# Optimization experiments

Hardware: AMD Instinct MI355X
Metric: run time of the kernel (lower is better)

## Reference

```python
import jax, jax.numpy as jnp
import numpy as np

B, S, E = 2, 4096, 512

def setup_inputs() -> dict:
    key = jax.random.key(0)
    kx, kq, kk, kv, ko = jax.random.split(key, 5)
    scale = 1.0 / np.sqrt(E)  # init-style scaling for weights
    return {
        "x": jax.random.normal(kx, (B, S, E), dtype=jnp.float32),
        "Wq": jax.random.normal(kq, (E, E), dtype=jnp.float32) * scale,
        "Wk": jax.random.normal(kk, (E, E), dtype=jnp.float32) * scale,
        "Wv": jax.random.normal(kv, (E, E), dtype=jnp.float32) * scale,
        "Wo": jax.random.normal(ko, (E, E), dtype=jnp.float32) * scale,
        "bo": jnp.zeros((E,), dtype=jnp.float32),
    }

def reference(x, Wq, Wk, Wv, Wo, bo):
    # nn.Linear: y = x @ W.T  (weights stored [out, in])
    q = jnp.einsum("bse,fe->bsf", x, Wq)
    k = jnp.einsum("bse,fe->bsf", x, Wk)
    v = jnp.einsum("bse,fe->bsf", x, Wv)
    inv_scale = 1.0 / jnp.sqrt(jnp.asarray(x.shape[-1], x.dtype))
    scores = jnp.einsum("bqe,bke->bqk", q, k) * inv_scale  # [B,S,S]
    S_len = x.shape[1]
    # torch.triu(ones) keeps j >= i; masked_fill where triu==0 masks j < i
    row = jnp.arange(S_len)[:, None]
    col = jnp.arange(S_len)[None, :]
    keep = col >= row  # [S,S], faithfully anti-causal as in the source
    scores = jnp.where(keep[None, :, :], scores, jnp.asarray(-jnp.inf, scores.dtype))
    attn = jax.nn.softmax(scores, axis=-1)
    # dropout p=0.0 -> identity
    out = jnp.einsum("bqk,bke->bqe", attn, v)
    return jnp.einsum("bse,fe->bsf", out, Wo) + bo
```

## Files before the change

### kernel.cpp

```cpp
#include <hip/hip_runtime.h>
#include <hip/hip_bf16.h>

#define S_LEN 4096
#define E_DIM 512
#define B_DIM 2
#define M_ROWS (B_DIM * S_LEN)

typedef __attribute__((ext_vector_type(8))) short short8;
typedef __attribute__((ext_vector_type(4))) float floatx4;

__device__ __forceinline__ unsigned short f2bf(float f) {
    unsigned u = __float_as_uint(f);
    unsigned r = (u + 0x7fffu + ((u >> 16) & 1u)) >> 16;
    return (unsigned short)r;
}
__device__ __forceinline__ float bf2f(unsigned short u) {
    return __uint_as_float((unsigned)u << 16);
}

__device__ __forceinline__ void async_copy16(unsigned short* lds, const unsigned short* g) {
    auto gp = (const __attribute__((address_space(1))) unsigned int*)g;
    auto lp = (__attribute__((address_space(3))) unsigned int*)lds;
    __builtin_amdgcn_global_load_lds(gp, lp, 16, 0, 0);
}

struct MapArg { unsigned short m[320]; };

__global__ __launch_bounds__(256) void convert_bf16(
    const float* __restrict__ x,  const float* __restrict__ wq,
    const float* __restrict__ wk, const float* __restrict__ wv,
    const float* __restrict__ wo, unsigned short* __restrict__ dst)
{
    long i = (long)blockIdx.x * 1024 + (long)threadIdx.x * 4;
    const float* src; long off;
    if      (i < 4194304) { src = x;  off = i; }
    else if (i < 4456448) { src = wq; off = i - 4194304; }
    else if (i < 4718592) { src = wk; off = i - 4456448; }
    else if (i < 4980736) { src = wv; off = i - 4718592; }
    else                  { src = wo; off = i - 4980736; }
    float4 v = *(const float4*)(src + off);
    ushort4 o;
    o.x = f2bf(v.x); o.y = f2bf(v.y); o.z = f2bf(v.z); o.w = f2bf(v.w);
    *(ushort4*)(dst + i) = o;
}

__device__ __forceinline__ void gemm_core(
    const unsigned short* __restrict__ A, const unsigned short* __restrict__ W,
    void* __restrict__ Cv, const float* __restrict__ bias, int mode,
    int m0, int n0)
{
    __shared__ unsigned short As[128 * 32];
    __shared__ unsigned short Bs[128 * 32];
    const int tid = threadIdx.x;
    const int lane = tid & 63, wave = tid >> 6;
    const int wm = wave >> 1, wn = wave & 1;
    const int q4 = lane >> 4, l16 = lane & 15;

    floatx4 acc[4][4];
#pragma unroll
    for (int i = 0; i < 4; ++i)
#pragma unroll
        for (int j = 0; j < 4; ++j) acc[i][j] = (floatx4){0.f, 0.f, 0.f, 0.f};

    const int srow = lane >> 2;
    const int scol = (lane & 3) * 8;

    for (int k0 = 0; k0 < 512; k0 += 32) {
        async_copy16(&As[(wave * 16) * 32],
                     A + (size_t)(m0 + wave * 16 + srow) * 512 + k0 + scol);
        async_copy16(&As[(64 + wave * 16) * 32],
                     A + (size_t)(m0 + 64 + wave * 16 + srow) * 512 + k0 + scol);
        async_copy16(&Bs[(wave * 16) * 32],
                     W + (size_t)(n0 + wave * 16 + srow) * 512 + k0 + scol);
        async_copy16(&Bs[(64 + wave * 16) * 32],
                     W + (size_t)(n0 + 64 + wave * 16 + srow) * 512 + k0 + scol);
        __syncthreads();
        short8 af[4], bfr[4];
#pragma unroll
        for (int i = 0; i < 4; ++i) {
            af[i]  = *(const short8*)&As[(wm * 64 + i * 16 + l16) * 32 + q4 * 8];
            bfr[i] = *(const short8*)&Bs[(wn * 64 + i * 16 + l16) * 32 + q4 * 8];
        }
#pragma unroll
        for (int i = 0; i < 4; ++i)
#pragma unroll
            for (int j = 0; j < 4; ++j)
                acc[i][j] = __builtin_amdgcn_mfma_f32_16x16x32_bf16(af[i], bfr[j], acc[i][j], 0, 0, 0);
        __syncthreads();
    }

    if (mode == 0) {
        unsigned short* C = (unsigned short*)Cv;
#pragma unroll
        for (int i = 0; i < 4; ++i) {
            int rowb = m0 + wm * 64 + i * 16 + q4 * 4;
#pragma unroll
            for (int j = 0; j < 4; ++j) {
                int col = n0 + wn * 64 + j * 16 + l16;
#pragma unroll
                for (int rg = 0; rg < 4; ++rg)
                    C[(size_t)(rowb + rg) * 512 + col] = f2bf(acc[i][j][rg]);
            }
        }
    } else if (mode == 1) {
        unsigned short* C = (unsigned short*)Cv;
#pragma unroll
        for (int i = 0; i < 4; ++i) {
            int grow = m0 + wm * 64 + i * 16 + q4 * 4;
            int b = grow >> 12, s = grow & 4095;
#pragma unroll
            for (int j = 0; j < 4; ++j) {
                int e = n0 + wn * 64 + j * 16 + l16;
                ushort4 pk;
                pk.x = f2bf(acc[i][j][0]); pk.y = f2bf(acc[i][j][1]);
                pk.z = f2bf(acc[i][j][2]); pk.w = f2bf(acc[i][j][3]);
                *(ushort4*)(C + (size_t)b * 512 * 4096 + (size_t)e * 4096 + s) = pk;
            }
        }
    } else {
        float* C = (float*)Cv;
#pragma unroll
        for (int i = 0; i < 4; ++i) {
            int rowb = m0 + wm * 64 + i * 16 + q4 * 4;
#pragma unroll
            for (int j = 0; j < 4; ++j) {
                int col = n0 + wn * 64 + j * 16 + l16;
                float bv = bias[col];
#pragma unroll
                for (int rg = 0; rg < 4; ++rg)
                    C[(size_t)(rowb + rg) * 512 + col] = acc[i][j][rg] + bv;
            }
        }
    }
}

__global__ __launch_bounds__(256) void gemm_qkv(
    const unsigned short* __restrict__ xb,
    const unsigned short* __restrict__ Wqb, const unsigned short* __restrict__ Wkb,
    const unsigned short* __restrict__ Wvb,
    unsigned short* __restrict__ Qb, unsigned short* __restrict__ Kb,
    unsigned short* __restrict__ Vtb)
{
    const int z = blockIdx.z;
    const unsigned short* W = (z == 0) ? Wqb : (z == 1) ? Wkb : Wvb;
    unsigned short* C = (z == 0) ? Qb : (z == 1) ? Kb : Vtb;
    gemm_core(xb, W, C, nullptr, (z == 2) ? 1 : 0, blockIdx.y * 128, blockIdx.x * 128);
}

__global__ __launch_bounds__(256) void gemm_out(
    const unsigned short* __restrict__ AOb, const unsigned short* __restrict__ Wob,
    const float* __restrict__ bo, float* __restrict__ out)
{
    gemm_core(AOb, Wob, out, bo, 2, blockIdx.y * 128, blockIdx.x * 128);
}

__global__ __launch_bounds__(512, 2) void flash_mfma(
    const unsigned short* __restrict__ Qg, const unsigned short* __restrict__ Kg,
    const unsigned short* __restrict__ Vt,
    unsigned short* __restrict__ Oh, float* __restrict__ Lb, MapArg map)
{
    const int enc = map.m[blockIdx.x];
    const int tile = enc & 63, ch = (enc >> 6) & 3, bb = enc >> 8;
    const int i0 = tile * 64;
    const int lo0 = 1024 * ch, hi = 1024 * ch + 1024;
    const int lo = (i0 > lo0) ? i0 : lo0;

    const int tid = threadIdx.x;
    const int lane = tid & 63, w = tid >> 6;
    const int s = w & 3, h = w >> 2;
    const int q4 = lane >> 4, l16 = lane & 15;
    const float scale = 0.044194173824159216f;
    const float MREF = 4.0f;

    __shared__ float Sred[4][64][36];
    __shared__ unsigned short Plds[64][40];
    __shared__ float Lred[64][8];

    const size_t rowbase = (size_t)bb * S_LEN;
    const size_t vbase   = (size_t)bb * 512 * 4096;

    short8 aq[4][4];
#pragma unroll
    for (int mg = 0; mg < 4; ++mg)
#pragma unroll
        for (int ks = 0; ks < 4; ++ks)
            aq[mg][ks] = *(const short8*)(Qg + (rowbase + i0 + mg * 16 + l16) * 512
                                          + s * 128 + ks * 32 + q4 * 8);

    floatx4 oacc[4][4];
#pragma unroll
    for (int mg = 0; mg < 4; ++mg)
#pragma unroll
        for (int nc = 0; nc < 4; ++nc) oacc[mg][nc] = (floatx4){0.f, 0.f, 0.f, 0.f};

    const int r = tid >> 3;
    const int g = tid & 7;
    float l_acc = 0.f;

    auto step = [&](int j0, short8 (&bkc)[4], short8 (&bkn)[4], int jn) {
        short8 vf[4];
#pragma unroll
        for (int nc = 0; nc < 4; ++nc)
            vf[nc] = *(const short8*)(Vt + vbase
                + (size_t)(w * 64 + nc * 16 + l16) * 4096 + j0 + q4 * 8);
#pragma unroll
        for (int ks = 0; ks < 4; ++ks)
            bkn[ks] = *(const short8*)(Kg + (rowbase + jn + h * 16 + l16) * 512
                                       + s * 128 + ks * 32 + q4 * 8);
        floatx4 sf[4];
#pragma unroll
        for (int mg = 0; mg < 4; ++mg) sf[mg] = (floatx4){0.f, 0.f, 0.f, 0.f};
#pragma unroll
        for (int ks = 0; ks < 4; ++ks)
#pragma unroll
            for (int mg = 0; mg < 4; ++mg)
                sf[mg] = __builtin_amdgcn_mfma_f32_16x16x32_bf16(
                    bkc[ks], aq[mg][ks], sf[mg], 0, 0, 0);
#pragma unroll
        for (int mg = 0; mg < 4; ++mg)
            *(floatx4*)&Sred[s][mg * 16 + l16][h * 16 + q4 * 4] = sf[mg];
        __syncthreads();

        float4 a0 = *(const float4*)&Sred[0][r][4 * g];
        float4 a1 = *(const float4*)&Sred[1][r][4 * g];
        float4 a2 = *(const float4*)&Sred[2][r][4 * g];
        float4 a3 = *(const float4*)&Sred[3][r][4 * g];
        float sv[4] = { a0.x + a1.x + a2.x + a3.x, a0.y + a1.y + a2.y + a3.y,
                        a0.z + a1.z + a2.z + a3.z, a0.w + a1.w + a2.w + a3.w };
        ushort4 pk;
        float p0, p1, p2, p3;
        {
            int key = j0 + 4 * g;
            int row = i0 + r;
            p0 = (key + 0 >= row) ? __expf(sv[0] * scale - MREF) : 0.f;
            p1 = (key + 1 >= row) ? __expf(sv[1] * scale - MREF) : 0.f;
            p2 = (key + 2 >= row) ? __expf(sv[2] * scale - MREF) : 0.f;
            p3 = (key + 3 >= row) ? __expf(sv[3] * scale - MREF) : 0.f;
        }
        l_acc += p0 + p1 + p2 + p3;
        pk.x = f2bf(p0); pk.y = f2bf(p1); pk.z = f2bf(p2); pk.w = f2bf(p3);
        *(ushort4*)&Plds[r][4 * g] = pk;
        __syncthreads();

        short8 ap[4];
#pragma unroll
        for (int mg = 0; mg < 4; ++mg)
            ap[mg] = *(const short8*)&Plds[mg * 16 + l16][q4 * 8];
#pragma unroll
        for (int mg = 0; mg < 4; ++mg)
#pragma unroll
            for (int nc = 0; nc < 4; ++nc)
                oacc[mg][nc] = __builtin_amdgcn_mfma_f32_16x16x32_bf16(
                    ap[mg], vf[nc], oacc[mg][nc], 0, 0, 0);
    };

    short8 bkA[4], bkB[4];
    int j0 = hi - 32;
#pragma unroll
    for (int ks = 0; ks < 4; ++ks)
        bkA[ks] = *(const short8*)(Kg + (rowbase + j0 + h * 16 + l16) * 512
                                   + s * 128 + ks * 32 + q4 * 8);
    while (j0 >= lo) {
        int jn = (j0 - 32 >= lo) ? j0 - 32 : lo;
        step(j0, bkA, bkB, jn);
        j0 -= 32;
        if (j0 < lo) break;
        jn = (j0 - 32 >= lo) ? j0 - 32 : lo;
        step(j0, bkB, bkA, jn);
        j0 -= 32;
    }
    __syncthreads();

    const int baseArr = (ch == 0) ? 0 : (ch == 1) ? 32 : (ch == 2) ? 96 : 192;
    const int slot = baseArr + bb * 16 * (ch + 1) + tile;

    Lred[r][g] = l_acc;
    __syncthreads();
    if (tid < 64) {
        float sum = 0.f;
#pragma unroll
        for (int gg = 0; gg < 8; ++gg) sum += Lred[tid][gg];
        Lb[(size_t)slot * 64 + tid] = sum;
    }

    unsigned short* Op = Oh + (size_t)slot * 64 * 512;
#pragma unroll
    for (int mg = 0; mg < 4; ++mg)
#pragma unroll
        for (int nc = 0; nc < 4; ++nc)
#pragma unroll
            for (int rg = 0; rg < 4; ++rg)
                Op[(size_t)(mg * 16 + q4 * 4 + rg) * 512 + w * 64 + nc * 16 + l16]
                    = f2bf(oacc[mg][nc][rg]);
}

__global__ __launch_bounds__(256) void flash_merge(
    const unsigned short* __restrict__ Oh, const float* __restrict__ Lb,
    unsigned short* __restrict__ AO)
{
    const int row = blockIdx.x;
    const int c = threadIdx.x * 2;
    const int bb = row >> 12, i = row & 4095;
    const int t = i >> 6, ri = i & 63;
    const int chmin = i >> 10;
    float lsum = 0.f, v0 = 0.f, v1 = 0.f;
#pragma unroll
    for (int ch = 0; ch < 4; ++ch) {
        if (ch < chmin) continue;
        int baseArr = (ch == 0) ? 0 : (ch == 1) ? 32 : (ch == 2) ? 96 : 192;
        int slot = baseArr + bb * 16 * (ch + 1) + t;
        lsum += Lb[(size_t)slot * 64 + ri];
        const unsigned short* p = Oh + (size_t)slot * 64 * 512 + (size_t)ri * 512 + c;
        v0 += bf2f(p[0]);
        v1 += bf2f(p[1]);
    }
    float inv = 1.f / lsum;
    ushort2 o; o.x = f2bf(v0 * inv); o.y = f2bf(v1 * inv);
    *(ushort2*)(AO + (size_t)row * 512 + c) = o;
}

static MapArg build_map() {
    int enc[320], steps[320], n = 0;
    for (int bb = 0; bb < 2; ++bb)
        for (int ch = 0; ch < 4; ++ch)
            for (int t = 0; t < 16 * (ch + 1) && t < 64; ++t) {
                int i0 = t * 64, lo0 = 1024 * ch, hi = lo0 + 1024;
                int lo = (i0 > lo0) ? i0 : lo0;
                enc[n] = t | (ch << 6) | (bb << 8);
                steps[n] = (hi - lo) / 32;
                ++n;
            }
    for (int i = 1; i < n; ++i) {
        int e = enc[i], st = steps[i], j = i - 1;
        while (j >= 0 && steps[j] > st) {
            steps[j + 1] = steps[j]; enc[j + 1] = enc[j]; --j;
        }
        steps[j + 1] = st; enc[j + 1] = e;
    }
    MapArg mp{};
    for (int c = 0; c < 64; ++c) {
        mp.m[c]       = (unsigned short)enc[127 - c];
        mp.m[256 + c] = (unsigned short)enc[c];
    }
    for (int k = 0; k < 192; ++k)
        mp.m[64 + k] = (unsigned short)enc[128 + k];
    return mp;
}

extern "C" void kernel_launch(void* const* d_in, const int* in_sizes, int n_in,
                              void* d_out, int out_size, void* d_ws, size_t ws_size,
                              hipStream_t stream) {
    (void)in_sizes; (void)n_in; (void)out_size; (void)ws_size;
    const float* x  = (const float*)d_in[0];
    const float* Wq = (const float*)d_in[1];
    const float* Wk = (const float*)d_in[2];
    const float* Wv = (const float*)d_in[3];
    const float* Wo = (const float*)d_in[4];
    const float* bo = (const float*)d_in[5];
    float* out = (float*)d_out;

    unsigned short* xb  = (unsigned short*)d_ws;
    unsigned short* Wqb = xb  + 4194304;
    unsigned short* Wkb = Wqb + 262144;
    unsigned short* Wvb = Wkb + 262144;
    unsigned short* Wob = Wvb + 262144;
    unsigned short* Qb  = Wob + 262144;
    unsigned short* Kb  = Qb  + 4194304;
    unsigned short* Vtb = Kb  + 4194304;
    unsigned short* AOb = Vtb + 4194304;
    unsigned short* Ohb = AOb + 4194304;
    float* Lbf = (float*)(Ohb + 10485760);

    static const MapArg mp = build_map();

    convert_bf16<<<5120, 256, 0, stream>>>(x, Wq, Wk, Wv, Wo, xb);

    gemm_qkv<<<dim3(4, 64, 3), 256, 0, stream>>>(xb, Wqb, Wkb, Wvb, Qb, Kb, Vtb);

    flash_mfma<<<320, 512, 0, stream>>>(Qb, Kb, Vtb, Ohb, Lbf, mp);

    flash_merge<<<8192, 256, 0, stream>>>(Ohb, Lbf, AOb);

    gemm_out<<<dim3(4, 64), 256, 0, stream>>>(AOb, Wob, bo, out);
}
```

Measured before the change: 231.7 us.

## Halve flash query tile to 32 rows and double block count

Shrinks the attention query tile from 64 to 32 rows, doubling the grid to 640 blocks, and raises launch_bounds occupancy to 4 blocks per CU. It also drops the K double-buffered prefetch in favour of a simple loop, and rebuilds the work map with a descending sort and serpentine assignment for load balance. This aims to fill the 256 CUs better and cut the tail imbalance. The cost is that each K/V tile is loaded twice as often per query row, and K loads are no longer prefetched.

```diff
diff --git a/kernel.cpp b/kernel.cpp
--- a/kernel.cpp
+++ b/kernel.cpp
@@ -24,7 +24,7 @@
     __builtin_amdgcn_global_load_lds(gp, lp, 16, 0, 0);
 }
 
-struct MapArg { unsigned short m[320]; };
+struct MapArg { unsigned short m[640]; };
 
 __global__ __launch_bounds__(256) void convert_bf16(
     const float* __restrict__ x,  const float* __restrict__ wq,
@@ -154,14 +154,14 @@
     gemm_core(AOb, Wob, out, bo, 2, blockIdx.y * 128, blockIdx.x * 128);
 }
 
-__global__ __launch_bounds__(512, 2) void flash_mfma(
+__global__ __launch_bounds__(512, 4) void flash_mfma(
     const unsigned short* __restrict__ Qg, const unsigned short* __restrict__ Kg,
     const unsigned short* __restrict__ Vt,
     unsigned short* __restrict__ Oh, float* __restrict__ Lb, MapArg map)
 {
     const int enc = map.m[blockIdx.x];
-    const int tile = enc & 63, ch = (enc >> 6) & 3, bb = enc >> 8;
-    const int i0 = tile * 64;
+    const int tile = enc & 127, ch = (enc >> 7) & 3, bb = enc >> 9;
+    const int i0 = tile * 32;
     const int lo0 = 1024 * ch, hi = 1024 * ch + 1024;
     const int lo = (i0 > lo0) ? i0 : lo0;
 
@@ -172,120 +172,101 @@
     const float scale = 0.044194173824159216f;
     const float MREF = 4.0f;
 
-    __shared__ float Sred[4][64][36];
-    __shared__ unsigned short Plds[64][40];
-    __shared__ float Lred[64][8];
+    __shared__ float Sred[4][32][36];
+    __shared__ unsigned short Plds[32][40];
+    __shared__ float Lred[32][16];
 
     const size_t rowbase = (size_t)bb * S_LEN;
     const size_t vbase   = (size_t)bb * 512 * 4096;
 
-    short8 aq[4][4];
-#pragma unroll
-    for (int mg = 0; mg < 4; ++mg)
-#pragma unroll
-        for (int ks = 0; ks < 4; ++ks)
-            aq[mg][ks] = *(const short8*)(Qg + (rowbase + i0 + mg * 16 + l16) * 512
-                                          + s * 128 + ks * 32 + q4 * 8);
-
-    floatx4 oacc[4][4];
-#pragma unroll
-    for (int mg = 0; mg < 4; ++mg)
+    short8 aq[2][4];
+#pragma unroll
+    for (int mg = 0; mg < 2; ++mg)
+#pragma unroll
+        for (int kd = 0; kd < 4; ++kd)
+            aq[mg][kd] = *(const short8*)(Qg + (rowbase + i0 + mg * 16 + l16) * 512
+                                          + s * 128 + kd * 32 + q4 * 8);
+
+    floatx4 oacc[2][4];
+#pragma unroll
+    for (int mg = 0; mg < 2; ++mg)
 #pragma unroll
         for (int nc = 0; nc < 4; ++nc) oacc[mg][nc] = (floatx4){0.f, 0.f, 0.f, 0.f};
 
-    const int r = tid >> 3;
-    const int g = tid & 7;
+    const int r = tid >> 4;
+    const int g = tid & 15;
     float l_acc = 0.f;
 
-    auto step = [&](int j0, short8 (&bkc)[4], short8 (&bkn)[4], int jn) {
-        short8 vf[4];
+    for (int j0 = hi - 32; j0 >= lo; j0 -= 32) {
+        short8 bk[4], vf[4];
+#pragma unroll
+        for (int kd = 0; kd < 4; ++kd)
+            bk[kd] = *(const short8*)(Kg + (rowbase + j0 + h * 16 + l16) * 512
+                                      + s * 128 + kd * 32 + q4 * 8);
 #pragma unroll
         for (int nc = 0; nc < 4; ++nc)
             vf[nc] = *(const short8*)(Vt + vbase
                 + (size_t)(w * 64 + nc * 16 + l16) * 4096 + j0 + q4 * 8);
-#pragma unroll
-        for (int ks = 0; ks < 4; ++ks)
-            bkn[ks] = *(const short8*)(Kg + (rowbase + jn + h * 16 + l16) * 512
-                                       + s * 128 + ks * 32 + q4 * 8);
-        floatx4 sf[4];
-#pragma unroll
-        for (int mg = 0; mg < 4; ++mg) sf[mg] = (floatx4){0.f, 0.f, 0.f, 0.f};
-#pragma unroll
-        for (int ks = 0; ks < 4; ++ks)
-#pragma unroll
-            for (int mg = 0; mg < 4; ++mg)
+
+        floatx4 sf[2];
+#pragma unroll
+        for (int mg = 0; mg < 2; ++mg) sf[mg] = (floatx4){0.f, 0.f, 0.f, 0.f};
+#pragma unroll
+        for (int kd = 0; kd < 4; ++kd)
+#pragma unroll
+            for (int mg = 0; mg < 2; ++mg)
                 sf[mg] = __builtin_amdgcn_mfma_f32_16x16x32_bf16(
-                    bkc[ks], aq[mg][ks], sf[mg], 0, 0, 0);
-#pragma unroll
-        for (int mg = 0; mg < 4; ++mg)
+                    bk[kd], aq[mg][kd], sf[mg], 0, 0, 0);
+#pragma unroll
+        for (int mg = 0; mg < 2; ++mg)
             *(floatx4*)&Sred[s][mg * 16 + l16][h * 16 + q4 * 4] = sf[mg];
         __syncthreads();
 
-        float4 a0 = *(const float4*)&Sred[0][r][4 * g];
-        float4 a1 = *(const float4*)&Sred[1][r][4 * g];
-        float4 a2 = *(const float4*)&Sred[2][r][4 * g];
-        float4 a3 = *(const float4*)&Sred[3][r][4 * g];
-        float sv[4] = { a0.x + a1.x + a2.x + a3.x, a0.y + a1.y + a2.y + a3.y,
-                        a0.z + a1.z + a2.z + a3.z, a0.w + a1.w + a2.w + a3.w };
-        ushort4 pk;
-        float p0, p1, p2, p3;
+        float sv0, sv1;
         {
-            int key = j0 + 4 * g;
-            int row = i0 + r;
-            p0 = (key + 0 >= row) ? __expf(sv[0] * scale - MREF) : 0.f;
-            p1 = (key + 1 >= row) ? __expf(sv[1] * scale - MREF) : 0.f;
-            p2 = (key + 2 >= row) ? __expf(sv[2] * scale - MREF) : 0.f;
-            p3 = (key + 3 >= row) ? __expf(sv[3] * scale - MREF) : 0.f;
-        }
-        l_acc += p0 + p1 + p2 + p3;
-        pk.x = f2bf(p0); pk.y = f2bf(p1); pk.z = f2bf(p2); pk.w = f2bf(p3);
-        *(ushort4*)&Plds[r][4 * g] = pk;
+            float2 a0 = *(const float2*)&Sred[0][r][2 * g];
+            float2 a1 = *(const float2*)&Sred[1][r][2 * g];
+            float2 a2 = *(const float2*)&Sred[2][r][2 * g];
+            float2 a3 = *(const float2*)&Sred[3][r][2 * g];
+            sv0 = a0.x + a1.x + a2.x + a3.x;
+            sv1 = a0.y + a1.y + a2.y + a3.y;
+        }
+        int key = j0 + 2 * g, row = i0 + r;
+        float p0 = (key + 0 >= row) ? __expf(sv0 * scale - MREF) : 0.f;
+        float p1 = (key + 1 >= row) ? __expf(sv1 * scale - MREF) : 0.f;
+        l_acc += p0 + p1;
+        ushort2 pk; pk.x = f2bf(p0); pk.y = f2bf(p1);
+        *(ushort2*)&Plds[r][2 * g] = pk;
         __syncthreads();
 
-        short8 ap[4];
-#pragma unroll
-        for (int mg = 0; mg < 4; ++mg)
+        short8 ap[2];
+#pragma unroll
+        for (int mg = 0; mg < 2; ++mg)
             ap[mg] = *(const short8*)&Plds[mg * 16 + l16][q4 * 8];
 #pragma unroll
-        for (int mg = 0; mg < 4; ++mg)
+        for (int mg = 0; mg < 2; ++mg)
 #pragma unroll
             for (int nc = 0; nc < 4; ++nc)
                 oacc[mg][nc] = __builtin_amdgcn_mfma_f32_16x16x32_bf16(
                     ap[mg], vf[nc], oacc[mg][nc], 0, 0, 0);
-    };
-
-    short8 bkA[4], bkB[4];
-    int j0 = hi - 32;
-#pragma unroll
-    for (int ks = 0; ks < 4; ++ks)
-        bkA[ks] = *(const short8*)(Kg + (rowbase + j0 + h * 16 + l16) * 512
-                                   + s * 128 + ks * 32 + q4 * 8);
-    while (j0 >= lo) {
-        int jn = (j0 - 32 >= lo) ? j0 - 32 : lo;
-        step(j0, bkA, bkB, jn);
-        j0 -= 32;
-        if (j0 < lo) break;
-        jn = (j0 - 32 >= lo) ? j0 - 32 : lo;
-        step(j0, bkB, bkA, jn);
-        j0 -= 32;
     }
     __syncthreads();
 
     const int baseArr = (ch == 0) ? 0 : (ch == 1) ? 32 : (ch == 2) ? 96 : 192;
-    const int slot = baseArr + bb * 16 * (ch + 1) + tile;
+    const int slot = bb * 320 + baseArr + tile;
 
     Lred[r][g] = l_acc;
     __syncthreads();
-    if (tid < 64) {
+    if (tid < 32) {
         float sum = 0.f;
 #pragma unroll
-        for (int gg = 0; gg < 8; ++gg) sum += Lred[tid][gg];
-        Lb[(size_t)slot * 64 + tid] = sum;
-    }
-
-    unsigned short* Op = Oh + (size_t)slot * 64 * 512;
-#pragma unroll
-    for (int mg = 0; mg < 4; ++mg)
+        for (int gg = 0; gg < 16; ++gg) sum += Lred[tid][gg];
+        Lb[(size_t)slot * 32 + tid] = sum;
+    }
+
+    unsigned short* Op = Oh + (size_t)slot * 32 * 512;
+#pragma unroll
+    for (int mg = 0; mg < 2; ++mg)
 #pragma unroll
         for (int nc = 0; nc < 4; ++nc)
 #pragma unroll
@@ -301,16 +282,16 @@
     const int row = blockIdx.x;
     const int c = threadIdx.x * 2;
     const int bb = row >> 12, i = row & 4095;
-    const int t = i >> 6, ri = i & 63;
+    const int t = i >> 5, ri = i & 31;
     const int chmin = i >> 10;
     float lsum = 0.f, v0 = 0.f, v1 = 0.f;
 #pragma unroll
     for (int ch = 0; ch < 4; ++ch) {
         if (ch < chmin) continue;
         int baseArr = (ch == 0) ? 0 : (ch == 1) ? 32 : (ch == 2) ? 96 : 192;
-        int slot = baseArr + bb * 16 * (ch + 1) + t;
-        lsum += Lb[(size_t)slot * 64 + ri];
-        const unsigned short* p = Oh + (size_t)slot * 64 * 512 + (size_t)ri * 512 + c;
+        int slot = bb * 320 + baseArr + t;
+        lsum += Lb[(size_t)slot * 32 + ri];
+        const unsigned short* p = Oh + (size_t)slot * 32 * 512 + (size_t)ri * 512 + c;
         v0 += bf2f(p[0]);
         v1 += bf2f(p[1]);
     }
@@ -320,30 +301,30 @@
 }
 
 static MapArg build_map() {
-    int enc[320], steps[320], n = 0;
+    int enc[640], steps[640], n = 0;
     for (int bb = 0; bb < 2; ++bb)
         for (int ch = 0; ch < 4; ++ch)
-            for (int t = 0; t < 16 * (ch + 1) && t < 64; ++t) {
-                int i0 = t * 64, lo0 = 1024 * ch, hi = lo0 + 1024;
+            for (int t = 0; t < 128; ++t) {
+                int i0 = 32 * t, lo0 = 1024 * ch, hi = lo0 + 1024;
+                if (i0 >= hi) continue;
                 int lo = (i0 > lo0) ? i0 : lo0;
-                enc[n] = t | (ch << 6) | (bb << 8);
+                enc[n] = t | (ch << 7) | (bb << 9);
                 steps[n] = (hi - lo) / 32;
                 ++n;
             }
     for (int i = 1; i < n; ++i) {
         int e = enc[i], st = steps[i], j = i - 1;
-        while (j >= 0 && steps[j] > st) {
+        while (j >= 0 && steps[j] < st) {
             steps[j + 1] = steps[j]; enc[j + 1] = enc[j]; --j;
         }
         steps[j + 1] = st; enc[j + 1] = e;
     }
     MapArg mp{};
-    for (int c = 0; c < 64; ++c) {
-        mp.m[c]       = (unsigned short)enc[127 - c];
-        mp.m[256 + c] = (unsigned short)enc[c];
-    }
-    for (int k = 0; k < 192; ++k)
-        mp.m[64 + k] = (unsigned short)enc[128 + k];
+    for (int k = 0; k < n; ++k) {
+        int r = k >> 8, c = k & 255;
+        int b = (r & 1) ? (r * 256 + (255 - c)) : (r * 256 + c);
+        mp.m[b] = (unsigned short)enc[k];
+    }
     return mp;
 }
 
@@ -377,7 +358,7 @@
 
     gemm_qkv<<<dim3(4, 64, 3), 256, 0, stream>>>(xb, Wqb, Wkb, Wvb, Qb, Kb, Vtb);
 
-    flash_mfma<<<320, 512, 0, stream>>>(Qb, Kb, Vtb, Ohb, Lbf, mp);
+    flash_mfma<<<640, 512, 0, stream>>>(Qb, Kb, Vtb, Ohb, Lbf, mp);
 
     flash_merge<<<8192, 256, 0, stream>>>(Ohb, Lbf, AOb);
 
```

Result: slower. 276.5 us (+19.4%).
